# Optimization experiments

Hardware: AMD Instinct MI355X
Metric: run time of the kernel (lower is better)

## Reference

```python
import jax, jax.numpy as jnp
import numpy as np

NUM_USERS = 100000
NUM_ITEMS = 200000
EMBED_DIM = 128
NUM_EDGES = 2000000
N_LAYERS = 2
EPS = 1e-5


def layer_norm(x, gamma, beta):
    m = jnp.mean(x, axis=-1, keepdims=True)
    v = jnp.mean(jnp.square(x - m), axis=-1, keepdims=True)
    return gamma * (x - m) * jax.lax.rsqrt(v + EPS) + beta


def setup_inputs() -> dict:
    key = jax.random.key(0)
    k1, k2, k3, k4, k5 = jax.random.split(key, 5)
    user_emb = jax.random.normal(k1, (NUM_USERS, EMBED_DIM), dtype=jnp.float32) * 0.1
    item_emb = jax.random.normal(k2, (NUM_ITEMS, EMBED_DIM), dtype=jnp.float32) * 0.1
    # COO edge list for the user-item bipartite graph; iu_adj = ui_adj^T
    rows = jax.random.randint(k3, (NUM_EDGES,), 0, NUM_USERS, dtype=jnp.int32)
    cols = jax.random.randint(k4, (NUM_EDGES,), 0, NUM_ITEMS, dtype=jnp.int32)
    # positive normalized edge weights (e.g. sym-normalized adjacency values)
    vals = jax.random.uniform(k5, (NUM_EDGES,), dtype=jnp.float32) * (1.0 / 16.0)
    ln_gamma = jnp.ones((EMBED_DIM,), dtype=jnp.float32)
    ln_beta = jnp.zeros((EMBED_DIM,), dtype=jnp.float32)
    return {"user_emb": user_emb, "item_emb": item_emb, "vals": vals,
            "ln_gamma": ln_gamma, "ln_beta": ln_beta, "rows": rows, "cols": cols}


def reference(user_emb, item_emb, vals, ln_gamma, ln_beta, rows, cols):
    # SpMM via gather + segment_sum (COO). dropout is identity (eval / p=0).
    u_emb, i_emb = user_emb, item_emb
    for _ in range(N_LAYERS):
        # u_temp = ui_adj @ i_emb : [NUM_USERS, D]
        u_temp = jax.ops.segment_sum(vals[:, None] * i_emb[cols], rows,
                                     num_segments=NUM_USERS)
        # i_temp = iu_adj @ u_emb : [NUM_ITEMS, D]  (iu_adj = ui_adj^T)
        i_temp = jax.ops.segment_sum(vals[:, None] * u_emb[rows], cols,
                                     num_segments=NUM_ITEMS)
        u_emb = layer_norm(u_emb + u_temp, ln_gamma, ln_beta)
        i_emb = layer_norm(i_emb + i_temp, ln_gamma, ln_beta)
    return u_emb, i_emb
```

## Files before the change

### kernel.cpp

```cpp
#include <hip/hip_runtime.h>

#define EPS 1e-5f
typedef long long ll;
typedef unsigned int uint;
typedef float f32x2 __attribute__((ext_vector_type(2)));

#define CHUNK   4096
#define NCPAD   1024
#define NBMAX   2048
#define P3CAP   8192

__device__ __forceinline__ uint bf_round(float x) {
    uint u = __float_as_uint(x);
    return (u + 0x7FFFu + ((u >> 16) & 1u)) >> 16;
}
__device__ __forceinline__ uint pack2(float a, float b) {
    return bf_round(a) | (bf_round(b) << 16);
}
__device__ __forceinline__ float unpack_lo(uint u) { return __uint_as_float(u << 16); }
__device__ __forceinline__ float unpack_hi(uint u) { return __uint_as_float(u & 0xFFFF0000u); }

__global__ __launch_bounds__(256) void hist_conv_k(
    const int* __restrict__ rows, const int* __restrict__ cols,
    int* __restrict__ counts, int ne, int nu, int NB, int hb,
    const float* __restrict__ ue, const float* __restrict__ ie,
    uint4* __restrict__ bfout, int nuT, int totT)
{
    int b = blockIdx.x;
    if (b < hb) {
        __shared__ int hist[NBMAX];
        for (int i = threadIdx.x; i < NB; i += 256) hist[i] = 0;
        __syncthreads();
        ll base0 = (ll)b * CHUNK;
        ll items = 2LL * ne;
        int n2 = (int)min((ll)CHUNK, items - base0);
        for (int k = threadIdx.x; k < n2; k += 256) {
            ll e = base0 + k;
            int bucket = (e < ne) ? rows[e] : nu + cols[e - ne];
            atomicAdd(&hist[bucket >> 8], 1);
        }
        __syncthreads();
        for (int i = threadIdx.x; i < NB; i += 256)
            counts[(ll)i * NCPAD + b] = hist[i];
    } else {
        int t = (b - hb) * 256 + threadIdx.x;
        if (t < totT) {
            const float4* src = (t < nuT) ? (const float4*)(ue + (ll)t * 8)
                                          : (const float4*)(ie + (ll)(t - nuT) * 8);
            float4 f0 = src[0], f1 = src[1];
            uint4 q;
            q.x = pack2(f0.x, f0.y); q.y = pack2(f0.z, f0.w);
            q.z = pack2(f1.x, f1.y); q.w = pack2(f1.z, f1.w);
            bfout[t] = q;
        }
    }
}

__global__ __launch_bounds__(256) void s1_kernel(
    const int* __restrict__ counts, int* __restrict__ base,
    int* __restrict__ binT, int nchunk)
{
    int b = blockIdx.x;
    int t = threadIdx.x;
    int4 v = ((const int4*)(counts + (ll)b * NCPAD))[t];
    int i0 = 4 * t;
    if (i0 + 0 >= nchunk) v.x = 0;
    if (i0 + 1 >= nchunk) v.y = 0;
    if (i0 + 2 >= nchunk) v.z = 0;
    if (i0 + 3 >= nchunk) v.w = 0;
    int s = v.x + v.y + v.z + v.w;
    __shared__ int sm[256];
    sm[t] = s; __syncthreads();
    for (int off = 1; off < 256; off <<= 1) {
        int a = (t >= off) ? sm[t - off] : 0;
        __syncthreads();
        sm[t] += a;
        __syncthreads();
    }
    int excl = sm[t] - s;
    int4 o;
    o.x = excl; o.y = o.x + v.x; o.z = o.y + v.y; o.w = o.z + v.z;
    ((int4*)(base + (ll)b * NCPAD))[t] = o;
    if (t == 255) binT[b] = sm[255];
}

__global__ __launch_bounds__(256) void s2_kernel(
    const int* __restrict__ binT, int* __restrict__ binptr,
    int* __restrict__ rowptr, int NB, int Nrow, int total)
{
    __shared__ int sm[256];
    int t = threadIdx.x;
    const int PER = NBMAX / 256;
    int loc[PER]; int s = 0;
#pragma unroll
    for (int k = 0; k < PER; k++) {
        int i = t * PER + k;
        loc[k] = (i < NB) ? binT[i] : 0;
        s += loc[k];
    }
    sm[t] = s; __syncthreads();
    for (int off = 1; off < 256; off <<= 1) {
        int a = (t >= off) ? sm[t - off] : 0;
        __syncthreads();
        sm[t] += a;
        __syncthreads();
    }
    int run = sm[t] - s;
#pragma unroll
    for (int k = 0; k < PER; k++) {
        int i = t * PER + k;
        if (i < NB) binptr[i] = run;
        run += loc[k];
    }
    if (t == 0) { binptr[NB] = total; rowptr[Nrow] = total; }
}

__global__ __launch_bounds__(256) void p2_kernel(
    const int* __restrict__ rows, const int* __restrict__ cols,
    const float* __restrict__ vals,
    const int* __restrict__ base, const int* __restrict__ binptr,
    int2* __restrict__ tmp, int ne, int nu, int NB)
{
    __shared__ int cur[NBMAX];
    int c = blockIdx.x;
    for (int i = threadIdx.x; i < NB; i += 256)
        cur[i] = binptr[i] + base[(ll)i * NCPAD + c];
    __syncthreads();
    ll base0 = (ll)c * CHUNK;
    ll items = 2LL * ne;
    int n2 = (int)min((ll)CHUNK, items - base0);
    for (int k = threadIdx.x; k < n2; k += 256) {
        ll e = base0 + k;
        int bucket, src; float v;
        if (e < ne) { bucket = rows[e]; src = cols[e]; v = vals[e]; }
        else        { ll e2 = e - ne; bucket = nu + cols[e2]; src = rows[e2]; v = vals[e2]; }
        int slot = atomicAdd(&cur[bucket >> 8], 1);
        tmp[slot] = make_int2(((bucket & 255) << 24) | src, __float_as_int(v));
    }
}

__global__ __launch_bounds__(256) void p3_kernel(
    const int2* __restrict__ tmp, const int* __restrict__ binptr,
    int* __restrict__ rowptr, int2* __restrict__ csr)
{
    __shared__ int hist[256];
    __shared__ int sm[256];
    __shared__ int2 stage[P3CAP];
    int b = blockIdx.x;
    int t = threadIdx.x;
    int s0 = binptr[b], s1 = binptr[b + 1];
    int n = s1 - s0;
    bool inLds = (n <= P3CAP);
    hist[t] = 0; __syncthreads();
    if (inLds) {
        for (int i = t; i < n; i += 256) {
            int2 it = tmp[s0 + i];
            stage[i] = it;
            atomicAdd(&hist[(uint)it.x >> 24], 1);
        }
    } else {
        for (int i = t; i < n; i += 256)
            atomicAdd(&hist[(uint)tmp[s0 + i].x >> 24], 1);
    }
    __syncthreads();
    int v = hist[t];
    sm[t] = v; __syncthreads();
    for (int off = 1; off < 256; off <<= 1) {
        int a = (t >= off) ? sm[t - off] : 0;
        __syncthreads();
        sm[t] += a;
        __syncthreads();
    }
    int excl = sm[t] - v;
    __syncthreads();
    rowptr[(b << 8) + t] = s0 + excl;
    hist[t] = excl;
    __syncthreads();
    if (inLds) {
        for (int i = t; i < n; i += 256) {
            int2 it = stage[i];
            int r = atomicAdd(&hist[(uint)it.x >> 24], 1);
            csr[s0 + r] = make_int2(it.x & 0xFFFFFF, it.y);
        }
    } else {
        for (int i = t; i < n; i += 256) {
            int2 it = tmp[s0 + i];
            int r = atomicAdd(&hist[(uint)it.x >> 24], 1);
            csr[s0 + r] = make_int2(it.x & 0xFFFFFF, it.y);
        }
    }
}

template<bool OUT_BF>
__global__ __launch_bounds__(256) void gather_ln_k(
    const uint4* __restrict__ srcU,
    const uint4* __restrict__ srcI,
    const uint4* __restrict__ resU, const uint4* __restrict__ resI,
    void* __restrict__ outU, void* __restrict__ outI,
    const int* __restrict__ rowptr, const int2* __restrict__ csr,
    const float* __restrict__ gamma, const float* __restrict__ beta,
    int nu, int N)
{
    int gw = blockIdx.x * 4 + (threadIdx.x >> 6);
    if (gw * 4 >= N) return;
    int lane = threadIdx.x & 63;
    int sub  = lane >> 4;
    int l16  = lane & 15;

    int row = gw * 4 + sub;
    bool rv = row < N;
    int rowc = rv ? row : N - 1;

    int start = rv ? rowptr[row]     : 0;
    int end   = rv ? rowptr[row + 1] : 0;
    int deg   = end - start;
    int md = deg;
    md = max(md, __shfl_xor(md, 16, 64));
    md = max(md, __shfl_xor(md, 32, 64));

    const uint4* tbl;
    const uint4* res;
    char* outp;
    if (rowc < nu) {
        tbl  = srcU;
        res  = resU + (ll)rowc * 16;
        outp = OUT_BF ? (char*)outU + (ll)rowc * 256
                      : (char*)outU + (ll)rowc * 512;
    } else {
        int k = rowc - nu;
        tbl  = srcI;
        res  = resI + (ll)k * 16;
        outp = OUT_BF ? (char*)outI + (ll)k * 256
                      : (char*)outI + (ll)k * 512;
    }

    f32x2 a01 = {0.f, 0.f}, a23 = {0.f, 0.f}, a45 = {0.f, 0.f}, a67 = {0.f, 0.f};

#define FMA8(q, vv) {                                                   \
        f32x2 b;                                                        \
        b[0] = unpack_lo(q.x); b[1] = unpack_hi(q.x); a01 = vv * b + a01; \
        b[0] = unpack_lo(q.y); b[1] = unpack_hi(q.y); a23 = vv * b + a23; \
        b[0] = unpack_lo(q.z); b[1] = unpack_hi(q.z); a45 = vv * b + a45; \
        b[0] = unpack_lo(q.w); b[1] = unpack_hi(q.w); a67 = vv * b + a67; }

    if (md > 0) {
        int2 ec0 = csr[(0 < deg) ? start     : 0];
        int2 ec1 = csr[(1 < deg) ? start + 1 : 0];
        uint4 q0 = tbl[(((uint)ec0.x) << 4) + l16];
        for (int k = 0; k < md; ++k) {
            int2 ec2 = csr[((k + 2) < deg) ? (start + k + 2) : 0];
            uint4 q1 = tbl[(((uint)ec1.x) << 4) + l16];
            float vm = (k < deg) ? __int_as_float(ec0.y) : 0.0f;
            f32x2 vv = {vm, vm};
            FMA8(q0, vv);
            ec0 = ec1; ec1 = ec2; q0 = q1;
        }
    }
#undef FMA8

    float a0 = a01[0], a1 = a01[1], a2 = a23[0], a3 = a23[1];
    float a4 = a45[0], a5 = a45[1], a6 = a67[0], a7 = a67[1];

    uint4 r = res[l16];
    a0 += unpack_lo(r.x); a1 += unpack_hi(r.x);
    a2 += unpack_lo(r.y); a3 += unpack_hi(r.y);
    a4 += unpack_lo(r.z); a5 += unpack_hi(r.z);
    a6 += unpack_lo(r.w); a7 += unpack_hi(r.w);

    float s  = a0+a1+a2+a3+a4+a5+a6+a7;
    float ss = a0*a0+a1*a1+a2*a2+a3*a3+a4*a4+a5*a5+a6*a6+a7*a7;
#pragma unroll
    for (int off = 8; off > 0; off >>= 1) {
        s  += __shfl_xor(s, off, 64);
        ss += __shfl_xor(ss, off, 64);
    }
    float m   = s * (1.0f / 128.0f);
    float var = ss * (1.0f / 128.0f) - m * m;
    float inv = rsqrtf(var + EPS);

    float4 g0 = ((const float4*)gamma)[l16 * 2];
    float4 g1 = ((const float4*)gamma)[l16 * 2 + 1];
    float4 b0 = ((const float4*)beta)[l16 * 2];
    float4 b1 = ((const float4*)beta)[l16 * 2 + 1];
    float o0 = g0.x * (a0 - m) * inv + b0.x;
    float o1 = g0.y * (a1 - m) * inv + b0.y;
    float o2 = g0.z * (a2 - m) * inv + b0.z;
    float o3 = g0.w * (a3 - m) * inv + b0.w;
    float o4 = g1.x * (a4 - m) * inv + b1.x;
    float o5 = g1.y * (a5 - m) * inv + b1.y;
    float o6 = g1.z * (a6 - m) * inv + b1.z;
    float o7 = g1.w * (a7 - m) * inv + b1.w;

    if (rv) {
        if (OUT_BF) {
            uint4 q;
            q.x = pack2(o0, o1); q.y = pack2(o2, o3);
            q.z = pack2(o4, o5); q.w = pack2(o6, o7);
            ((uint4*)outp)[l16] = q;
        } else {
            ((float4*)outp)[l16 * 2]     = make_float4(o0, o1, o2, o3);
            ((float4*)outp)[l16 * 2 + 1] = make_float4(o4, o5, o6, o7);
        }
    }
}

extern "C" void kernel_launch(void* const* d_in, const int* in_sizes, int n_in,
                              void* d_out, int out_size, void* d_ws, size_t ws_size,
                              hipStream_t stream)
{
    const float* user_emb = (const float*)d_in[0];
    const float* item_emb = (const float*)d_in[1];
    const float* vals     = (const float*)d_in[2];
    const float* gamma    = (const float*)d_in[3];
    const float* beta     = (const float*)d_in[4];
    const int*   rows     = (const int*)d_in[5];
    const int*   cols     = (const int*)d_in[6];

    const int nu = in_sizes[0] / 128;
    const int ni = in_sizes[1] / 128;
    const int ne = in_sizes[2];
    const int N  = nu + ni;
    const int total = 2 * ne;

    float* dout   = (float*)d_out;
    float* dout_u = dout;
    float* dout_i = dout + (ll)nu * 128;

    uint* bf_u = (uint*)d_out;
    uint* bf_i = bf_u + (ll)nu * 64;

    const int NB = (N + 255) >> 8;
    const int hb = (total + CHUNK - 1) / CHUNK;

    int*  rowptr  = (int*)d_ws;
    int*  counts  = rowptr + (ll)NB * 256;
    int*  base    = counts + (ll)NB * NCPAD;
    int*  binT    = base + (ll)NB * NCPAD;
    int*  binptr  = binT + NBMAX;
    int2* csr     = (int2*)(binptr + NBMAX);
    uint* wu_out  = (uint*)(csr + total);
    uint* wi_out  = wu_out + (ll)nu * 64;
    int2* tmp     = (int2*)wu_out;

    const int totT = (nu + ni) * 16;
    const int tb   = (totT + 255) / 256;

    hist_conv_k<<<hb + tb, 256, 0, stream>>>(rows, cols, counts, ne, nu, NB, hb,
                                             user_emb, item_emb,
                                             (uint4*)bf_u, nu * 16, totT);
    s1_kernel<<<NB, 256, 0, stream>>>(counts, base, binT, hb);
    s2_kernel<<<1, 256, 0, stream>>>(binT, binptr, rowptr, NB, N, total);
    p2_kernel<<<hb, 256, 0, stream>>>(rows, cols, vals, base, binptr, tmp, ne, nu, NB);
    p3_kernel<<<NB, 256, 0, stream>>>(tmp, binptr, rowptr, csr);

    const int gblocks = (N + 15) / 16;

    gather_ln_k<true><<<gblocks, 256, 0, stream>>>(
        (const uint4*)bf_i, (const uint4*)bf_u,
        (const uint4*)bf_u, (const uint4*)bf_i,
        wu_out, wi_out,
        rowptr, csr, gamma, beta, nu, N);

    gather_ln_k<false><<<gblocks, 256, 0, stream>>>(
        (const uint4*)wi_out, (const uint4*)wu_out,
        (const uint4*)wu_out, (const uint4*)wi_out,
        dout_u, dout_i,
        rowptr, csr, gamma, beta, nu, N);
}
```

Baseline: 693.5 us.

## Deepen gather prefetch to two rows per iteration and double chunk size

```diff
diff --git a/kernel.cpp b/kernel.cpp
--- a/kernel.cpp
+++ b/kernel.cpp
@@ -5,8 +5,8 @@
 typedef unsigned int uint;
 typedef float f32x2 __attribute__((ext_vector_type(2)));
 
-#define CHUNK   4096
-#define NCPAD   1024
+#define CHUNK   8192
+#define NCPAD   512
 #define NBMAX   2048
 #define P3CAP   8192
 
@@ -62,13 +62,10 @@
 {
     int b = blockIdx.x;
     int t = threadIdx.x;
-    int4 v = ((const int4*)(counts + (ll)b * NCPAD))[t];
-    int i0 = 4 * t;
-    if (i0 + 0 >= nchunk) v.x = 0;
-    if (i0 + 1 >= nchunk) v.y = 0;
-    if (i0 + 2 >= nchunk) v.z = 0;
-    if (i0 + 3 >= nchunk) v.w = 0;
-    int s = v.x + v.y + v.z + v.w;
+    int i0 = 2 * t, i1 = 2 * t + 1;
+    int v0 = (i0 < nchunk) ? counts[(ll)b * NCPAD + i0] : 0;
+    int v1 = (i1 < nchunk) ? counts[(ll)b * NCPAD + i1] : 0;
+    int s = v0 + v1;
     __shared__ int sm[256];
     sm[t] = s; __syncthreads();
     for (int off = 1; off < 256; off <<= 1) {
@@ -78,9 +75,8 @@
         __syncthreads();
     }
     int excl = sm[t] - s;
-    int4 o;
-    o.x = excl; o.y = o.x + v.x; o.z = o.y + v.y; o.w = o.z + v.z;
-    ((int4*)(base + (ll)b * NCPAD))[t] = o;
+    base[(ll)b * NCPAD + i0] = excl;
+    base[(ll)b * NCPAD + i1] = excl + v0;
     if (t == 255) binT[b] = sm[255];
 }
 
@@ -234,30 +230,40 @@
                       : (char*)outI + (ll)k * 512;
     }
 
-    f32x2 a01 = {0.f, 0.f}, a23 = {0.f, 0.f}, a45 = {0.f, 0.f}, a67 = {0.f, 0.f};
-
-#define FMA8(q, vv) {                                                   \
-        f32x2 b;                                                        \
-        b[0] = unpack_lo(q.x); b[1] = unpack_hi(q.x); a01 = vv * b + a01; \
-        b[0] = unpack_lo(q.y); b[1] = unpack_hi(q.y); a23 = vv * b + a23; \
-        b[0] = unpack_lo(q.z); b[1] = unpack_hi(q.z); a45 = vv * b + a45; \
-        b[0] = unpack_lo(q.w); b[1] = unpack_hi(q.w); a67 = vv * b + a67; }
+    f32x2 e01 = {0.f,0.f}, e23 = {0.f,0.f}, e45 = {0.f,0.f}, e67 = {0.f,0.f};
+    f32x2 o01 = {0.f,0.f}, o23 = {0.f,0.f}, o45 = {0.f,0.f}, o67 = {0.f,0.f};
+
+#define FMA8(q, vv, A, B, C, D) {                                       \
+        f32x2 b_;                                                       \
+        b_[0] = unpack_lo(q.x); b_[1] = unpack_hi(q.x); A = vv * b_ + A; \
+        b_[0] = unpack_lo(q.y); b_[1] = unpack_hi(q.y); B = vv * b_ + B; \
+        b_[0] = unpack_lo(q.z); b_[1] = unpack_hi(q.z); C = vv * b_ + C; \
+        b_[0] = unpack_lo(q.w); b_[1] = unpack_hi(q.w); D = vv * b_ + D; }
 
     if (md > 0) {
         int2 ec0 = csr[(0 < deg) ? start     : 0];
         int2 ec1 = csr[(1 < deg) ? start + 1 : 0];
+        int2 ec2 = csr[(2 < deg) ? start + 2 : 0];
+        int2 ec3 = csr[(3 < deg) ? start + 3 : 0];
         uint4 q0 = tbl[(((uint)ec0.x) << 4) + l16];
-        for (int k = 0; k < md; ++k) {
-            int2 ec2 = csr[((k + 2) < deg) ? (start + k + 2) : 0];
-            uint4 q1 = tbl[(((uint)ec1.x) << 4) + l16];
-            float vm = (k < deg) ? __int_as_float(ec0.y) : 0.0f;
-            f32x2 vv = {vm, vm};
-            FMA8(q0, vv);
-            ec0 = ec1; ec1 = ec2; q0 = q1;
+        uint4 q1 = tbl[(((uint)ec1.x) << 4) + l16];
+        for (int k = 0; k < md; k += 2) {
+            int2 ec4 = csr[((k + 4) < deg) ? (start + k + 4) : 0];
+            int2 ec5 = csr[((k + 5) < deg) ? (start + k + 5) : 0];
+            uint4 q2 = tbl[(((uint)ec2.x) << 4) + l16];
+            uint4 q3 = tbl[(((uint)ec3.x) << 4) + l16];
+            float v0 = (k < deg)       ? __int_as_float(ec0.y) : 0.0f;
+            float v1 = ((k + 1) < deg) ? __int_as_float(ec1.y) : 0.0f;
+            f32x2 vv0 = {v0, v0}, vv1 = {v1, v1};
+            FMA8(q0, vv0, e01, e23, e45, e67);
+            FMA8(q1, vv1, o01, o23, o45, o67);
+            ec0 = ec2; ec1 = ec3; ec2 = ec4; ec3 = ec5;
+            q0 = q2; q1 = q3;
         }
     }
 #undef FMA8
 
+    f32x2 a01 = e01 + o01, a23 = e23 + o23, a45 = e45 + o45, a67 = e67 + o67;
     float a0 = a01[0], a1 = a01[1], a2 = a23[0], a3 = a23[1];
     float a4 = a45[0], a5 = a45[1], a6 = a67[0], a7 = a67[1];
 
```

Result: faster. 671.2 us (-3.2%).
